# Kernel optimization log

Measured on AMD Instinct MI355X. Metric: run time of the kernel, lower is better.

## Reference

```python
import jax, jax.numpy as jnp
from jax import lax
import numpy as np

B, H, W = 16, 512, 512
NBINS = 256
MARGIN_EYE = 12
BLUR_SIZE = 5
ALPHA_SKIN, ALPHA_EYE, ALPHA_LIP = 0.3, 0.8, 0.1


def de_norm(x):
    return jnp.clip((x + 1.0) * 0.5, 0.0, 1.0)


def renorm(x):
    return x * 2.0 - 1.0


def _match_channel(src, ref, w_s, w_r):
    # src/ref: (P,) pixel values in [0,255]; w_s/w_r: (P,) mask weights
    b_s = jnp.clip(src.astype(jnp.int32), 0, NBINS - 1)
    b_r = jnp.clip(ref.astype(jnp.int32), 0, NBINS - 1)
    h_s = jnp.zeros((NBINS,), src.dtype).at[b_s].add(w_s)   # masked histogram
    h_r = jnp.zeros((NBINS,), ref.dtype).at[b_r].add(w_r)
    cdf_s = jnp.cumsum(h_s) / jnp.maximum(jnp.sum(h_s), 1e-6)
    cdf_r = jnp.cumsum(h_r) / jnp.maximum(jnp.sum(h_r), 1e-6)
    # CDF-matching transfer table (equiv. of cal_trans in PSGAN/EleGANt)
    table = jnp.clip(jnp.searchsorted(cdf_r, cdf_s), 0, NBINS - 1).astype(src.dtype)
    return table[b_s]


def masked_his_match(image_s, image_r, mask_s, mask_r):
    # image: (3,H,W), mask: (1,H,W)
    s = de_norm(image_s) * 255.0 * mask_s
    r = de_norm(image_r) * 255.0 * mask_r
    w_s = mask_s.reshape(-1)
    w_r = mask_r.reshape(-1)
    matched = jax.vmap(_match_channel, in_axes=(0, 0, None, None))(
        s.reshape(3, -1), r.reshape(3, -1), w_s, w_r).reshape(s.shape)
    matched = jnp.where(mask_s > 0, matched, s)  # only masked pixels replaced
    return renorm(matched / 255.0)


def expand_area(mask, margin):
    # morphological dilation (max pool) of (1,H,W) mask
    k = 2 * margin + 1
    return lax.reduce_window(mask, 0.0, lax.max, (1, k, k), (1, 1, 1), 'SAME')


def mask_blur(mask, blur_size):
    # box blur; 'valid' mode: blurred support kept inside original mask
    k = blur_size
    s = lax.reduce_window(mask, 0.0, lax.add, (1, k, k), (1, 1, 1), 'SAME') / float(k * k)
    return s * mask


def generate_pgt(image_s, image_r, mask_s, mask_r, lms_s, lms_r):
    pgt = image_s
    # skin (channel 1)
    m = mask_s[1:2]
    pgt = (1.0 - m) * pgt + m * masked_his_match(image_s, image_r, m, mask_r[1:2])
    # neck (channel 4)
    m = mask_s[4:5]
    pgt = (1.0 - m) * pgt + m * masked_his_match(image_s, image_r, m, mask_r[4:5])
    # lip (channel 0)
    m = mask_s[0:1]
    pgt = (1.0 - m) * pgt + m * masked_his_match(image_s, image_r, m, mask_r[0:1])
    # eyes (channels 2,3), dilated and intersected with skin
    m_se = expand_area(jnp.sum(mask_s[2:4], axis=0, keepdims=True), MARGIN_EYE) * mask_s[1:2]
    m_re = expand_area(jnp.sum(mask_r[2:4], axis=0, keepdims=True), MARGIN_EYE) * mask_r[1:2]
    eye_match = masked_his_match(image_s, image_r, m_se, m_re)
    mb = mask_blur(m_se, BLUR_SIZE)
    pgt = (1.0 - mb) * pgt + mb * eye_match
    # fine_align (reconstructed, simplified: per-region alpha blend of reference,
    # landmark warp omitted -- helper source not provided)
    for m, a in ((mask_s[1:2], ALPHA_SKIN), (m_se, ALPHA_EYE), (mask_s[0:1], ALPHA_LIP)):
        pgt = (1.0 - a * m) * pgt + (a * m) * image_r
    return pgt


def setup_inputs() -> dict:
    key = jax.random.key(0)
    ks = jax.random.split(key, 6)
    sources = jax.random.uniform(ks[0], (B, 3, H, W), jnp.float32, -1.0, 1.0)
    targets = jax.random.uniform(ks[1], (B, 3, H, W), jnp.float32, -1.0, 1.0)
    mask_srcs = (jax.random.uniform(ks[2], (B, 5, H, W)) < 0.3).astype(jnp.float32)
    mask_tars = (jax.random.uniform(ks[3], (B, 5, H, W)) < 0.3).astype(jnp.float32)
    lms_srcs = jax.random.uniform(ks[4], (B, 68, 2), jnp.float32, 0.0, float(H))
    lms_tars = jax.random.uniform(ks[5], (B, 68, 2), jnp.float32, 0.0, float(H))
    return {"sources": sources, "targets": targets, "mask_srcs": mask_srcs,
            "mask_tars": mask_tars, "lms_srcs": lms_srcs, "lms_tars": lms_tars}


def reference(sources, targets, mask_srcs, mask_tars, lms_srcs, lms_tars):
    # vmap over batch replaces the per-sample Python loop of ComposePGT.forward
    return jax.vmap(generate_pgt)(sources, targets, mask_srcs, mask_tars, lms_srcs, lms_tars)
```

## Files before the change

kernel.cpp:

```cpp
#include <hip/hip_runtime.h>
#include <stdint.h>

#define BB 16
#define HH 512
#define WW 512
#define HW (HH*WW)
#define NB 256

#define YC 36
#define SROWS 64
#define MROWS 40
#define NYCH 15


__device__ __forceinline__ float denorm255(float x) {
    return fminf(fmaxf((x + 1.0f) * 0.5f, 0.0f), 1.0f) * 255.0f;
}
__device__ __forceinline__ float renorm_lut(int t) {
    return ((float)t / 255.0f) * 2.0f - 1.0f;
}
__device__ __forceinline__ uint32_t alignb(uint32_t hi, uint32_t lo, int r) {
    return (uint32_t)(((((uint64_t)hi) << 32) | lo) >> (8 * r));
}

__device__ __forceinline__ void hist4(int* h, uint32_t cw,
                                      float4 v0, float4 v1, float4 v2)
{
    float d0[4] = {denorm255(v0.x), denorm255(v0.y), denorm255(v0.z), denorm255(v0.w)};
    float d1[4] = {denorm255(v1.x), denorm255(v1.y), denorm255(v1.z), denorm255(v1.w)};
    float d2[4] = {denorm255(v2.x), denorm255(v2.y), denorm255(v2.z), denorm255(v2.w)};
    #pragma unroll
    for (int j = 0; j < 4; j++) {
        uint32_t pb = (cw >> (8 * j)) & 0xFFu;
        if (pb & 8u) {
            atomicAdd(&h[0 * NB + min((int)d0[j], 255)], 1);
            atomicAdd(&h[1 * NB + min((int)d1[j], 255)], 1);
            atomicAdd(&h[2 * NB + min((int)d2[j], 255)], 1);
        }
        if (pb & 16u) {
            atomicAdd(&h[3 * NB + min((int)d0[j], 255)], 1);
            atomicAdd(&h[4 * NB + min((int)d1[j], 255)], 1);
            atomicAdd(&h[5 * NB + min((int)d2[j], 255)], 1);
        }
        if (pb & 4u) {
            atomicAdd(&h[6 * NB + min((int)d0[j], 255)], 1);
            atomicAdd(&h[7 * NB + min((int)d1[j], 255)], 1);
            atomicAdd(&h[8 * NB + min((int)d2[j], 255)], 1);
        }
        int mei = (int)((pb >> 5) & 3u);
        if (mei) {
            float fm = (float)mei;
            atomicAdd(&h[ 9 * NB + min((int)(d0[j] * fm), 255)], mei);
            atomicAdd(&h[10 * NB + min((int)(d1[j] * fm), 255)], mei);
            atomicAdd(&h[11 * NB + min((int)(d2[j] * fm), 255)], mei);
        }
    }
}

__global__ void __launch_bounds__(256) fused_mask_kernel(
    const float* __restrict__ ms, const float* __restrict__ mr,
    const float* __restrict__ src, const float* __restrict__ tgt,
    uint32_t* __restrict__ C, uint32_t* __restrict__ mbs,
    int* __restrict__ hist)
{
    __shared__ uint32_t sHor[SROWS][128];
    __shared__ uint32_t sMse[MROWS][129];
    __shared__ int h[2][12 * NB];

    int blk  = (blockIdx.x & 7) * 60 + (blockIdx.x >> 3);
    int ych  = blk % NYCH;
    int sb   = blk / NYCH;
    int side = sb >> 4;
    int b    = sb & 15;
    int y0   = ych * YC;

    const float* base = (side ? mr : ms) + (size_t)b * 5 * HW;
    int r0 = threadIdx.x >> 5;
    int c  = threadIdx.x & 31;

    for (int i = threadIdx.x; i < 2 * 12 * NB; i += 256) ((int*)h)[i] = 0;

    for (int it = 0; it < 8; ++it) {
        int L  = r0 + 8 * it;
        int gy = y0 - 14 + L;
        bool inimg = (gy >= 0 && gy < HH);
        bool m1row = inimg && (L >= 12 && L < 52);
        bool owned = inimg && (L >= 14 && L < 50);

        float4 v[5][4];
        #pragma unroll
        for (int p = 0; p < 5; p++)
            #pragma unroll
            for (int j = 0; j < 4; j++) v[p][j] = make_float4(0.f, 0.f, 0.f, 0.f);

        if (inimg) {
            const float* rowp = base + (size_t)gy * WW + 16 * c;
            const float4* p2 = (const float4*)(rowp + 2 * (size_t)HW);
            const float4* p3 = (const float4*)(rowp + 3 * (size_t)HW);
            #pragma unroll
            for (int j = 0; j < 4; j++) { v[2][j] = p2[j]; v[3][j] = p3[j]; }
            if (m1row) {
                const float4* p1 = (const float4*)(rowp + (size_t)HW);
                #pragma unroll
                for (int j = 0; j < 4; j++) v[1][j] = p1[j];
            }
            if (owned) {
                const float4* p0 = (const float4*)(rowp);
                const float4* p4 = (const float4*)(rowp + 4 * (size_t)HW);
                #pragma unroll
                for (int j = 0; j < 4; j++) { v[0][j] = p0[j]; v[4][j] = p4[j]; }
            }
        }

        uint32_t Wd[4], E[4];
        #pragma unroll
        for (int j = 0; j < 4; j++) {
            uint32_t wc = 0;
            #pragma unroll
            for (int k = 0; k < 4; k++) {
                float a0 = (&v[0][j].x)[k];
                float a1 = (&v[1][j].x)[k];
                float a2 = (&v[2][j].x)[k];
                float a3 = (&v[3][j].x)[k];
                float a4 = (&v[4][j].x)[k];
                uint32_t e  = (uint32_t)(a2 + a3);
                uint32_t pb = (a0 > 0.f ? 4u : 0u) | (a1 > 0.f ? 8u : 0u)
                            | (a4 > 0.f ? 16u : 0u);
                wc |= (e | pb) << (8 * k);
            }
            Wd[j] = wc;
            E[j]  = wc & 0x03030303u;
        }

        uint32_t Lw[3], Rw[3];
        #pragma unroll
        for (int i = 0; i < 3; i++) {
            uint32_t lv = __shfl_up(E[i + 1], 1, 32);
            Lw[i] = (c == 0) ? 0u : lv;
            uint32_t rv = __shfl_down(E[i], 1, 32);
            Rw[i] = (c == 31) ? 0u : rv;
        }
        uint32_t arr[10] = {Lw[0], Lw[1], Lw[2], E[0], E[1], E[2], E[3],
                            Rw[0], Rw[1], Rw[2]};
        #pragma unroll
        for (int k = 0; k < 4; k++) {
            const int b3 = 3 + k;
            uint32_t a = arr[b3];
            #pragma unroll
            for (int s = 1; s <= 12; s++) {
                int ai = s >> 2, rrs = s & 3;
                uint32_t vp, vm;
                if (rrs == 0) {
                    vp = arr[b3 + ai];
                    vm = arr[b3 - ai];
                } else {
                    vp = alignb(arr[b3 + ai + 1], arr[b3 + ai], rrs);
                    int am = (s + 3) >> 2;
                    vm = alignb(arr[b3 - am + 1], arr[b3 - am], 4 - rrs);
                }
                a |= vp | vm;
            }
            sHor[L][4 * c + k] = Wd[k] | (a << 5);
        }
    }
    __syncthreads();

    {
        int w  = threadIdx.x & 127;
        int mg = threadIdx.x >> 7;
        for (int k = 0; k < 20; ++k) {
            int m = mg * 20 + k;
            uint32_t o = 0;
            #pragma unroll
            for (int dy = 0; dy < 25; ++dy) o |= sHor[m + dy][w];
            uint32_t vv = (o >> 5) & 0x03030303u;
            uint32_t t3 = vv & (vv >> 1) & 0x01010101u;
            vv -= t3;
            uint32_t m1 = (sHor[m + 12][w] >> 3) & 0x01010101u;
            vv &= m1 * 3u;
            sMse[m][w] = vv;
        }
    }
    __syncthreads();

    {
        int ck = threadIdx.x & 31;
        int rr = threadIdx.x >> 5;
        size_t plane = (size_t)(side * BB + b);
        uint32_t* Cp = C + plane * (HW / 4);
        uint32_t* Mp = mbs + (size_t)b * (HW / 4);
        for (int o = rr; o < YC; o += 8) {
            int gy = y0 + o;
            if (gy >= HH) break;
            uint4 cw;
            #pragma unroll
            for (int q = 0; q < 4; q++) {
                uint32_t b5 = sHor[14 + o][4 * ck + q] & 0x1F1F1F1Fu;
                uint32_t mv = sMse[o + 2][4 * ck + q];
                (&cw.x)[q] = b5 | (mv << 5);
            }
            *((uint4*)(Cp + (size_t)gy * 128 + 4 * ck)) = cw;

            if (side == 0) {
                uint32_t s[6] = {0u, 0u, 0u, 0u, 0u, 0u};
                #pragma unroll
                for (int dy = 0; dy < 5; dy++) {
                    const uint32_t* rp = sMse[o + dy];
                    if (ck > 0)  s[0] += rp[4 * ck - 1];
                    s[1] += rp[4 * ck + 0];
                    s[2] += rp[4 * ck + 1];
                    s[3] += rp[4 * ck + 2];
                    s[4] += rp[4 * ck + 3];
                    if (ck < 31) s[5] += rp[4 * ck + 4];
                }
                uint4 ob;
                #pragma unroll
                for (int k = 0; k < 4; k++) {
                    uint32_t vv = s[k + 1];
                    vv += alignb(s[k + 1], s[k],     2);
                    vv += alignb(s[k + 1], s[k],     3);
                    vv += alignb(s[k + 2], s[k + 1], 1);
                    vv += alignb(s[k + 2], s[k + 1], 2);
                    (&ob.x)[k] = vv;
                }
                *((uint4*)(Mp + (size_t)gy * 128 + 4 * ck)) = ob;
            }
        }
    }

    {
        int* hw = h[threadIdx.x >> 7];
        const float* img = (side ? tgt : src) + (size_t)b * 3 * HW;
        const float4* i0 = (const float4*)(img);
        const float4* i1 = (const float4*)(img + HW);
        const float4* i2 = (const float4*)(img + 2 * (size_t)HW);
        for (int idx = threadIdx.x; idx < YC * 64; idx += 256) {
            int o = idx >> 6, g = idx & 63;
            int gy = y0 + o;
            if (gy >= HH) continue;
            int cidx = gy * 64 + g;
            uint32_t cwx = (sHor[14 + o][2 * g]     & 0x1F1F1F1Fu)
                         | (sMse[o + 2][2 * g]     << 5);
            uint32_t cwy = (sHor[14 + o][2 * g + 1] & 0x1F1F1F1Fu)
                         | (sMse[o + 2][2 * g + 1] << 5);
            float4 a0 = i0[2 * cidx], b0v = i0[2 * cidx + 1];
            float4 a1 = i1[2 * cidx], b1v = i1[2 * cidx + 1];
            float4 a2 = i2[2 * cidx], b2v = i2[2 * cidx + 1];
            hist4(hw, cwx, a0, a1, a2);
            hist4(hw, cwy, b0v, b1v, b2v);
        }
    }
    __syncthreads();
    {
        int* gh = hist + (size_t)(b * 2 + side) * 12 * NB;
        for (int i = threadIdx.x; i < 12 * NB; i += 256) {
            int s = h[0][i] + h[1][i];
            if (s) atomicAdd(&gh[i], s);
        }
    }
}

__global__ void __launch_bounds__(NB) table_kernel(
    const int* __restrict__ hist, uint8_t* __restrict__ table)
{
    int idx = blockIdx.x;
    int c = idx % 3; int rest = idx / 3; int rg = rest & 3; int b = rest >> 2;
    const int* hs = hist + ((size_t)((b * 2 + 0) * 4 + rg) * 3 + c) * NB;
    const int* hr = hist + ((size_t)((b * 2 + 1) * 4 + rg) * 3 + c) * NB;
    __shared__ int a[NB];
    __shared__ float cr[NB];
    int t = threadIdx.x;

    a[t] = hs[t];
    __syncthreads();
    for (int off = 1; off < NB; off <<= 1) {
        int v = (t >= off) ? a[t - off] : 0;
        __syncthreads();
        a[t] += v;
        __syncthreads();
    }
    int totS = a[NB - 1];
    int cumS = a[t];
    __syncthreads();

    a[t] = hr[t];
    __syncthreads();
    for (int off = 1; off < NB; off <<= 1) {
        int v = (t >= off) ? a[t - off] : 0;
        __syncthreads();
        a[t] += v;
        __syncthreads();
    }
    int totR = a[NB - 1];
    cr[t] = (float)a[t] / fmaxf((float)totR, 1e-6f);
    float v = (float)cumS / fmaxf((float)totS, 1e-6f);
    __syncthreads();

    int cnt = 0;
    for (int j = 0; j < NB; j++) cnt += (cr[j] < v) ? 1 : 0;
    table[(size_t)idx * NB + t] = (uint8_t)min(cnt, 255);
}

__device__ __forceinline__ void proc4(uint32_t cw, uint32_t qw,
    float4 x0, float4 x1, float4 x2, float4 r0, float4 r1, float4 r2,
    const uint8_t* tb, float4& o0, float4& o1, float4& o2)
{
    float X0[4] = {x0.x, x0.y, x0.z, x0.w};
    float X1[4] = {x1.x, x1.y, x1.z, x1.w};
    float X2[4] = {x2.x, x2.y, x2.z, x2.w};
    float R0[4] = {r0.x, r0.y, r0.z, r0.w};
    float R1[4] = {r1.x, r1.y, r1.z, r1.w};
    float R2[4] = {r2.x, r2.y, r2.z, r2.w};
    #pragma unroll
    for (int j = 0; j < 4; j++) {
        uint32_t pb = (cw >> (8 * j)) & 0xFFu;
        float q = (float)((qw >> (8 * j)) & 0xFFu);
        float m0f = (float)((pb >> 2) & 1u);
        float m1f = (float)((pb >> 3) & 1u);
        float m4f = (float)((pb >> 4) & 1u);
        float fm  = (float)((pb >> 5) & 3u);
        float d0 = denorm255(X0[j]), d1 = denorm255(X1[j]), d2 = denorm255(X2[j]);
        float p0 = X0[j], p1 = X1[j], p2 = X2[j];
        {
            float e0 = renorm_lut(tb[0 * NB + min((int)(d0 * m1f), 255)]);
            float e1 = renorm_lut(tb[1 * NB + min((int)(d1 * m1f), 255)]);
            float e2 = renorm_lut(tb[2 * NB + min((int)(d2 * m1f), 255)]);
            p0 = (1.0f - m1f) * p0 + m1f * e0;
            p1 = (1.0f - m1f) * p1 + m1f * e1;
            p2 = (1.0f - m1f) * p2 + m1f * e2;
        }
        {
            float e0 = renorm_lut(tb[3 * NB + min((int)(d0 * m4f), 255)]);
            float e1 = renorm_lut(tb[4 * NB + min((int)(d1 * m4f), 255)]);
            float e2 = renorm_lut(tb[5 * NB + min((int)(d2 * m4f), 255)]);
            p0 = (1.0f - m4f) * p0 + m4f * e0;
            p1 = (1.0f - m4f) * p1 + m4f * e1;
            p2 = (1.0f - m4f) * p2 + m4f * e2;
        }
        {
            float e0 = renorm_lut(tb[6 * NB + min((int)(d0 * m0f), 255)]);
            float e1 = renorm_lut(tb[7 * NB + min((int)(d1 * m0f), 255)]);
            float e2 = renorm_lut(tb[8 * NB + min((int)(d2 * m0f), 255)]);
            p0 = (1.0f - m0f) * p0 + m0f * e0;
            p1 = (1.0f - m0f) * p1 + m0f * e1;
            p2 = (1.0f - m0f) * p2 + m0f * e2;
        }
        {
            float mb = (q * (1.0f / 25.0f)) * fm;
            float e0 = renorm_lut(tb[ 9 * NB + min((int)(d0 * fm), 255)]);
            float e1 = renorm_lut(tb[10 * NB + min((int)(d1 * fm), 255)]);
            float e2 = renorm_lut(tb[11 * NB + min((int)(d2 * fm), 255)]);
            p0 = (1.0f - mb) * p0 + mb * e0;
            p1 = (1.0f - mb) * p1 + mb * e1;
            p2 = (1.0f - mb) * p2 + mb * e2;
        }
        float a = 0.3f * m1f;
        p0 = (1.0f - a) * p0 + a * R0[j];
        p1 = (1.0f - a) * p1 + a * R1[j];
        p2 = (1.0f - a) * p2 + a * R2[j];
        a = 0.8f * fm;
        p0 = (1.0f - a) * p0 + a * R0[j];
        p1 = (1.0f - a) * p1 + a * R1[j];
        p2 = (1.0f - a) * p2 + a * R2[j];
        a = 0.1f * m0f;
        p0 = (1.0f - a) * p0 + a * R0[j];
        p1 = (1.0f - a) * p1 + a * R1[j];
        p2 = (1.0f - a) * p2 + a * R2[j];
        (&o0.x)[j] = p0; (&o1.x)[j] = p1; (&o2.x)[j] = p2;
    }
}

__global__ void __launch_bounds__(256) compose_kernel(
    const float* __restrict__ src, const float* __restrict__ tgt,
    const uint32_t* __restrict__ C, const uint32_t* __restrict__ mbs,
    const uint8_t* __restrict__ table, float* __restrict__ out)
{
    int t = blockIdx.x * 256 + threadIdx.x;
    int b = t >> 15;
    int c = t & 32767;

    __shared__ uint8_t tb[12 * NB];
    {
        const uint32_t* gt = (const uint32_t*)(table + (size_t)b * 12 * NB);
        uint32_t* tw = (uint32_t*)tb;
        for (int i = threadIdx.x; i < 12 * NB / 4; i += 256) tw[i] = gt[i];
    }
    __syncthreads();

    const float4* s0 = (const float4*)(src + (size_t)b * 3 * HW);
    const float4* s1 = s0 + HW / 4;
    const float4* s2 = s1 + HW / 4;
    const float4* t0 = (const float4*)(tgt + (size_t)b * 3 * HW);
    const float4* t1 = t0 + HW / 4;
    const float4* t2 = t1 + HW / 4;
    const uint2* pc = (const uint2*)(C + (size_t)b * (HW / 4));
    const uint2* qc = (const uint2*)(mbs + (size_t)b * (HW / 4));
    float4* o0 = (float4*)(out + (size_t)b * 3 * HW);
    float4* o1 = o0 + HW / 4;
    float4* o2 = o1 + HW / 4;

    uint2 cw = pc[c];
    uint2 qw = qc[c];
    float4 xa0 = s0[2 * c], xb0 = s0[2 * c + 1];
    float4 xa1 = s1[2 * c], xb1 = s1[2 * c + 1];
    float4 xa2 = s2[2 * c], xb2 = s2[2 * c + 1];
    float4 ra0 = t0[2 * c], rb0 = t0[2 * c + 1];
    float4 ra1 = t1[2 * c], rb1 = t1[2 * c + 1];
    float4 ra2 = t2[2 * c], rb2 = t2[2 * c + 1];

    float4 oa0, oa1, oa2, ob0, ob1, ob2;
    proc4(cw.x, qw.x, xa0, xa1, xa2, ra0, ra1, ra2, tb, oa0, oa1, oa2);
    proc4(cw.y, qw.y, xb0, xb1, xb2, rb0, rb1, rb2, tb, ob0, ob1, ob2);

    o0[2 * c] = oa0; o0[2 * c + 1] = ob0;
    o1[2 * c] = oa1; o1[2 * c + 1] = ob1;
    o2[2 * c] = oa2; o2[2 * c + 1] = ob2;
}

extern "C" void kernel_launch(void* const* d_in, const int* in_sizes, int n_in,
                              void* d_out, int out_size, void* d_ws, size_t ws_size,
                              hipStream_t stream) {
    const float* src = (const float*)d_in[0];
    const float* tgt = (const float*)d_in[1];
    const float* ms  = (const float*)d_in[2];
    const float* mr  = (const float*)d_in[3];
    float* out = (float*)d_out;

    uint8_t* ws = (uint8_t*)d_ws;
    uint32_t* C   = (uint32_t*)(ws);
    uint32_t* mbs = (uint32_t*)(ws + (size_t)4 * BB * HW);
    int* hist     = (int*)(ws + (size_t)5 * BB * HW);
    uint8_t* table = ws + (size_t)5 * BB * HW + (size_t)2 * BB * 12 * NB * 4;

    hipMemsetAsync(hist, 0, (size_t)2 * BB * 12 * NB * sizeof(int), stream);

    fused_mask_kernel<<<2 * BB * NYCH, 256, 0, stream>>>(ms, mr, src, tgt, C, mbs, hist);
    table_kernel<<<BB * 4 * 3, NB, 0, stream>>>(hist, table);
    compose_kernel<<<BB * (HW / 8) / 256, 256, 0, stream>>>(src, tgt, C, mbs, table, out);
}
```

Baseline: 327.3 us.

## Software-pipeline image loads for histogram with inline-asm prefetch across barriers

Image float4 loads for the histogram phase are now issued with inline-asm global_load_dwordx4, before the vertical mask pass. They are double-buffered across the nine histogram steps using explicit vmcnt waits, so global-load latency overlaps with the LDS dilation work. The histogram phase moves ahead of the C/mask-blur write phase. __syncthreads is replaced by raw s_barrier with lgkmcnt waits. sMse padding changes so rows can be read as uint2. This adds register pressure and relies on hand-counted vmcnt values, which is fragile if the compiler inserts other memory ops.

Measured after the change: 334.9 us. 2.3% more time.

```diff
diff --git a/kernel.cpp b/kernel.cpp
--- a/kernel.cpp
+++ b/kernel.cpp
@@ -10,7 +10,10 @@
 #define YC 36
 #define SROWS 64
 #define MROWS 40
+#define MPAD 132
 #define NYCH 15
+
+typedef float f32x4 __attribute__((ext_vector_type(4)));
 
 
 __device__ __forceinline__ float denorm255(float x) {
@@ -24,35 +27,35 @@
 }
 
 __device__ __forceinline__ void hist4(int* h, uint32_t cw,
-                                      float4 v0, float4 v1, float4 v2)
+                                      f32x4 v0, f32x4 v1, f32x4 v2)
 {
-    float d0[4] = {denorm255(v0.x), denorm255(v0.y), denorm255(v0.z), denorm255(v0.w)};
-    float d1[4] = {denorm255(v1.x), denorm255(v1.y), denorm255(v1.z), denorm255(v1.w)};
-    float d2[4] = {denorm255(v2.x), denorm255(v2.y), denorm255(v2.z), denorm255(v2.w)};
     #pragma unroll
     for (int j = 0; j < 4; j++) {
         uint32_t pb = (cw >> (8 * j)) & 0xFFu;
+        float d0 = denorm255(v0[j]);
+        float d1 = denorm255(v1[j]);
+        float d2 = denorm255(v2[j]);
         if (pb & 8u) {
-            atomicAdd(&h[0 * NB + min((int)d0[j], 255)], 1);
-            atomicAdd(&h[1 * NB + min((int)d1[j], 255)], 1);
-            atomicAdd(&h[2 * NB + min((int)d2[j], 255)], 1);
+            atomicAdd(&h[0 * NB + min((int)d0, 255)], 1);
+            atomicAdd(&h[1 * NB + min((int)d1, 255)], 1);
+            atomicAdd(&h[2 * NB + min((int)d2, 255)], 1);
         }
         if (pb & 16u) {
-            atomicAdd(&h[3 * NB + min((int)d0[j], 255)], 1);
-            atomicAdd(&h[4 * NB + min((int)d1[j], 255)], 1);
-            atomicAdd(&h[5 * NB + min((int)d2[j], 255)], 1);
+            atomicAdd(&h[3 * NB + min((int)d0, 255)], 1);
+            atomicAdd(&h[4 * NB + min((int)d1, 255)], 1);
+            atomicAdd(&h[5 * NB + min((int)d2, 255)], 1);
         }
         if (pb & 4u) {
-            atomicAdd(&h[6 * NB + min((int)d0[j], 255)], 1);
-            atomicAdd(&h[7 * NB + min((int)d1[j], 255)], 1);
-            atomicAdd(&h[8 * NB + min((int)d2[j], 255)], 1);
+            atomicAdd(&h[6 * NB + min((int)d0, 255)], 1);
+            atomicAdd(&h[7 * NB + min((int)d1, 255)], 1);
+            atomicAdd(&h[8 * NB + min((int)d2, 255)], 1);
         }
         int mei = (int)((pb >> 5) & 3u);
         if (mei) {
             float fm = (float)mei;
-            atomicAdd(&h[ 9 * NB + min((int)(d0[j] * fm), 255)], mei);
-            atomicAdd(&h[10 * NB + min((int)(d1[j] * fm), 255)], mei);
-            atomicAdd(&h[11 * NB + min((int)(d2[j] * fm), 255)], mei);
+            atomicAdd(&h[ 9 * NB + min((int)(d0 * fm), 255)], mei);
+            atomicAdd(&h[10 * NB + min((int)(d1 * fm), 255)], mei);
+            atomicAdd(&h[11 * NB + min((int)(d2 * fm), 255)], mei);
         }
     }
 }
@@ -64,7 +67,7 @@
     int* __restrict__ hist)
 {
     __shared__ uint32_t sHor[SROWS][128];
-    __shared__ uint32_t sMse[MROWS][129];
+    __shared__ uint32_t sMse[MROWS][MPAD];
     __shared__ int h[2][12 * NB];
 
     int blk  = (blockIdx.x & 7) * 60 + (blockIdx.x >> 3);
@@ -77,6 +80,18 @@
     const float* base = (side ? mr : ms) + (size_t)b * 5 * HW;
     int r0 = threadIdx.x >> 5;
     int c  = threadIdx.x & 31;
+
+    int* hw = h[threadIdx.x >> 7];
+    const float* img = (side ? tgt : src) + (size_t)b * 3 * HW;
+    const float4* i0 = (const float4*)(img);
+    const float4* i1 = (const float4*)(img + HW);
+    const float4* i2 = (const float4*)(img + 2 * (size_t)HW);
+    auto cidx_of = [&](int it) -> int {
+        int idx = threadIdx.x + it * 256;
+        int o = idx >> 6, g = idx & 63;
+        int gyc = min(y0 + o, HH - 1);
+        return gyc * 64 + g;
+    };
 
     for (int i = threadIdx.x; i < 2 * 12 * NB; i += 256) ((int*)h)[i] = 0;
 
@@ -163,7 +178,25 @@
             sHor[L][4 * c + k] = Wd[k] | (a << 5);
         }
     }
-    __syncthreads();
+
+    f32x4 A0, A1, A2, A3, A4, A5, B0, B1, B2, B3, B4, B5;
+#define ISSUE(CIDX, R0, R1, R2, R3, R4, R5) do {                              \
+    int _ci = (CIDX);                                                         \
+    const float* _p0 = (const float*)(i0 + 2 * _ci);                          \
+    const float* _p1 = (const float*)(i1 + 2 * _ci);                          \
+    const float* _p2 = (const float*)(i2 + 2 * _ci);                          \
+    asm volatile("global_load_dwordx4 %0, %1, off"           : "=v"(R0) : "v"(_p0)); \
+    asm volatile("global_load_dwordx4 %0, %1, off offset:16" : "=v"(R1) : "v"(_p0)); \
+    asm volatile("global_load_dwordx4 %0, %1, off"           : "=v"(R2) : "v"(_p1)); \
+    asm volatile("global_load_dwordx4 %0, %1, off offset:16" : "=v"(R3) : "v"(_p1)); \
+    asm volatile("global_load_dwordx4 %0, %1, off"           : "=v"(R4) : "v"(_p2)); \
+    asm volatile("global_load_dwordx4 %0, %1, off offset:16" : "=v"(R5) : "v"(_p2)); \
+} while (0)
+    ISSUE(cidx_of(0), A0, A1, A2, A3, A4, A5);
+    ISSUE(cidx_of(1), B0, B1, B2, B3, B4, B5);
+
+    asm volatile("s_waitcnt lgkmcnt(0)" ::: "memory");
+    __builtin_amdgcn_s_barrier();
 
     {
         int w  = threadIdx.x & 127;
@@ -181,7 +214,33 @@
             sMse[m][w] = vv;
         }
     }
-    __syncthreads();
+    asm volatile("s_waitcnt lgkmcnt(0)" ::: "memory");
+    __builtin_amdgcn_s_barrier();
+
+#define STEP(IT, WAITN, R0, R1, R2, R3, R4, R5) do {                          \
+    asm volatile("s_waitcnt vmcnt(" WAITN ")" ::: "memory");                  \
+    __builtin_amdgcn_sched_barrier(0);                                        \
+    int _idx = threadIdx.x + (IT) * 256;                                      \
+    int _o = _idx >> 6, _g = _idx & 63;                                       \
+    if (y0 + _o < HH) {                                                       \
+        uint2 hv = *(const uint2*)&sHor[14 + _o][2 * _g];                     \
+        uint2 mv = *(const uint2*)&sMse[_o + 2][2 * _g];                      \
+        hist4(hw, (hv.x & 0x1F1F1F1Fu) | (mv.x << 5), R0, R2, R4);            \
+        hist4(hw, (hv.y & 0x1F1F1F1Fu) | (mv.y << 5), R1, R3, R5);            \
+    }                                                                         \
+    if ((IT) + 2 < 9) ISSUE(cidx_of((IT) + 2), R0, R1, R2, R3, R4, R5);       \
+} while (0)
+    STEP(0, "6", A0, A1, A2, A3, A4, A5);
+    STEP(1, "6", B0, B1, B2, B3, B4, B5);
+    STEP(2, "6", A0, A1, A2, A3, A4, A5);
+    STEP(3, "6", B0, B1, B2, B3, B4, B5);
+    STEP(4, "6", A0, A1, A2, A3, A4, A5);
+    STEP(5, "6", B0, B1, B2, B3, B4, B5);
+    STEP(6, "6", A0, A1, A2, A3, A4, A5);
+    STEP(7, "6", B0, B1, B2, B3, B4, B5);
+    STEP(8, "0", A0, A1, A2, A3, A4, A5);
+#undef STEP
+#undef ISSUE
 
     {
         int ck = threadIdx.x & 31;
@@ -228,29 +287,8 @@
         }
     }
 
-    {
-        int* hw = h[threadIdx.x >> 7];
-        const float* img = (side ? tgt : src) + (size_t)b * 3 * HW;
-        const float4* i0 = (const float4*)(img);
-        const float4* i1 = (const float4*)(img + HW);
-        const float4* i2 = (const float4*)(img + 2 * (size_t)HW);
-        for (int idx = threadIdx.x; idx < YC * 64; idx += 256) {
-            int o = idx >> 6, g = idx & 63;
-            int gy = y0 + o;
-            if (gy >= HH) continue;
-            int cidx = gy * 64 + g;
-            uint32_t cwx = (sHor[14 + o][2 * g]     & 0x1F1F1F1Fu)
-                         | (sMse[o + 2][2 * g]     << 5);
-            uint32_t cwy = (sHor[14 + o][2 * g + 1] & 0x1F1F1F1Fu)
-                         | (sMse[o + 2][2 * g + 1] << 5);
-            float4 a0 = i0[2 * cidx], b0v = i0[2 * cidx + 1];
-            float4 a1 = i1[2 * cidx], b1v = i1[2 * cidx + 1];
-            float4 a2 = i2[2 * cidx], b2v = i2[2 * cidx + 1];
-            hist4(hw, cwx, a0, a1, a2);
-            hist4(hw, cwy, b0v, b1v, b2v);
-        }
-    }
-    __syncthreads();
+    asm volatile("s_waitcnt lgkmcnt(0)" ::: "memory");
+    __builtin_amdgcn_s_barrier();
     {
         int* gh = hist + (size_t)(b * 2 + side) * 12 * NB;
         for (int i = threadIdx.x; i < 12 * NB; i += 256) {
```

## Halve row chunk per block and use single shared histogram for higher occupancy

Applied to the files above, without the earlier changes.

Cuts the rows each block owns from 36 to 18, so there are twice as many blocks (29 chunks per plane), and shrinks the shared arrays to match. The two per-half histogram copies are merged into one shared histogram, and sMse is padded to 132 so the mask words can be read as aligned uint2 loads. The aim is lower LDS use per block for better occupancy and balance, and fewer registers by denormalising pixel values lazily. The cost is a larger relative halo (the 14-row margin is recomputed more often) and more atomic contention on the single histogram.

Measured after the change: 331.7 us. No clear change (+1.3%).

```diff
diff --git a/kernel.cpp b/kernel.cpp
--- a/kernel.cpp
+++ b/kernel.cpp
@@ -7,10 +7,11 @@
 #define HW (HH*WW)
 #define NB 256
 
-#define YC 36
-#define SROWS 64
-#define MROWS 40
-#define NYCH 15
+#define YC 18
+#define SROWS 46
+#define MROWS 22
+#define MPAD 132
+#define NYCH 29
 
 
 __device__ __forceinline__ float denorm255(float x) {
@@ -26,33 +27,33 @@
 __device__ __forceinline__ void hist4(int* h, uint32_t cw,
                                       float4 v0, float4 v1, float4 v2)
 {
-    float d0[4] = {denorm255(v0.x), denorm255(v0.y), denorm255(v0.z), denorm255(v0.w)};
-    float d1[4] = {denorm255(v1.x), denorm255(v1.y), denorm255(v1.z), denorm255(v1.w)};
-    float d2[4] = {denorm255(v2.x), denorm255(v2.y), denorm255(v2.z), denorm255(v2.w)};
     #pragma unroll
     for (int j = 0; j < 4; j++) {
         uint32_t pb = (cw >> (8 * j)) & 0xFFu;
+        float d0 = denorm255((&v0.x)[j]);
+        float d1 = denorm255((&v1.x)[j]);
+        float d2 = denorm255((&v2.x)[j]);
         if (pb & 8u) {
-            atomicAdd(&h[0 * NB + min((int)d0[j], 255)], 1);
-            atomicAdd(&h[1 * NB + min((int)d1[j], 255)], 1);
-            atomicAdd(&h[2 * NB + min((int)d2[j], 255)], 1);
+            atomicAdd(&h[0 * NB + min((int)d0, 255)], 1);
+            atomicAdd(&h[1 * NB + min((int)d1, 255)], 1);
+            atomicAdd(&h[2 * NB + min((int)d2, 255)], 1);
         }
         if (pb & 16u) {
-            atomicAdd(&h[3 * NB + min((int)d0[j], 255)], 1);
-            atomicAdd(&h[4 * NB + min((int)d1[j], 255)], 1);
-            atomicAdd(&h[5 * NB + min((int)d2[j], 255)], 1);
+            atomicAdd(&h[3 * NB + min((int)d0, 255)], 1);
+            atomicAdd(&h[4 * NB + min((int)d1, 255)], 1);
+            atomicAdd(&h[5 * NB + min((int)d2, 255)], 1);
         }
         if (pb & 4u) {
-            atomicAdd(&h[6 * NB + min((int)d0[j], 255)], 1);
-            atomicAdd(&h[7 * NB + min((int)d1[j], 255)], 1);
-            atomicAdd(&h[8 * NB + min((int)d2[j], 255)], 1);
+            atomicAdd(&h[6 * NB + min((int)d0, 255)], 1);
+            atomicAdd(&h[7 * NB + min((int)d1, 255)], 1);
+            atomicAdd(&h[8 * NB + min((int)d2, 255)], 1);
         }
         int mei = (int)((pb >> 5) & 3u);
         if (mei) {
             float fm = (float)mei;
-            atomicAdd(&h[ 9 * NB + min((int)(d0[j] * fm), 255)], mei);
-            atomicAdd(&h[10 * NB + min((int)(d1[j] * fm), 255)], mei);
-            atomicAdd(&h[11 * NB + min((int)(d2[j] * fm), 255)], mei);
+            atomicAdd(&h[ 9 * NB + min((int)(d0 * fm), 255)], mei);
+            atomicAdd(&h[10 * NB + min((int)(d1 * fm), 255)], mei);
+            atomicAdd(&h[11 * NB + min((int)(d2 * fm), 255)], mei);
         }
     }
 }
@@ -64,10 +65,10 @@
     int* __restrict__ hist)
 {
     __shared__ uint32_t sHor[SROWS][128];
-    __shared__ uint32_t sMse[MROWS][129];
-    __shared__ int h[2][12 * NB];
-
-    int blk  = (blockIdx.x & 7) * 60 + (blockIdx.x >> 3);
+    __shared__ uint32_t sMse[MROWS][MPAD];
+    __shared__ int h[12 * NB];
+
+    int blk  = (blockIdx.x & 7) * 116 + (blockIdx.x >> 3);
     int ych  = blk % NYCH;
     int sb   = blk / NYCH;
     int side = sb >> 4;
@@ -78,14 +79,15 @@
     int r0 = threadIdx.x >> 5;
     int c  = threadIdx.x & 31;
 
-    for (int i = threadIdx.x; i < 2 * 12 * NB; i += 256) ((int*)h)[i] = 0;
-
-    for (int it = 0; it < 8; ++it) {
+    for (int i = threadIdx.x; i < 12 * NB; i += 256) h[i] = 0;
+
+    for (int it = 0; it < 6; ++it) {
         int L  = r0 + 8 * it;
+        if (L >= SROWS) break;
         int gy = y0 - 14 + L;
         bool inimg = (gy >= 0 && gy < HH);
-        bool m1row = inimg && (L >= 12 && L < 52);
-        bool owned = inimg && (L >= 14 && L < 50);
+        bool m1row = inimg && (L >= 12 && L < 34);
+        bool owned = inimg && (L >= 14 && L < 32);
 
         float4 v[5][4];
         #pragma unroll
@@ -168,8 +170,8 @@
     {
         int w  = threadIdx.x & 127;
         int mg = threadIdx.x >> 7;
-        for (int k = 0; k < 20; ++k) {
-            int m = mg * 20 + k;
+        for (int k = 0; k < 11; ++k) {
+            int m = mg * 11 + k;
             uint32_t o = 0;
             #pragma unroll
             for (int dy = 0; dy < 25; ++dy) o |= sHor[m + dy][w];
@@ -229,32 +231,31 @@
     }
 
     {
-        int* hw = h[threadIdx.x >> 7];
         const float* img = (side ? tgt : src) + (size_t)b * 3 * HW;
         const float4* i0 = (const float4*)(img);
         const float4* i1 = (const float4*)(img + HW);
         const float4* i2 = (const float4*)(img + 2 * (size_t)HW);
-        for (int idx = threadIdx.x; idx < YC * 64; idx += 256) {
+        for (int it = 0; it < 5; ++it) {
+            int idx = threadIdx.x + it * 256;
+            if (idx >= YC * 64) break;
             int o = idx >> 6, g = idx & 63;
             int gy = y0 + o;
             if (gy >= HH) continue;
             int cidx = gy * 64 + g;
-            uint32_t cwx = (sHor[14 + o][2 * g]     & 0x1F1F1F1Fu)
-                         | (sMse[o + 2][2 * g]     << 5);
-            uint32_t cwy = (sHor[14 + o][2 * g + 1] & 0x1F1F1F1Fu)
-                         | (sMse[o + 2][2 * g + 1] << 5);
+            uint2 hv = *(const uint2*)&sHor[14 + o][2 * g];
+            uint2 mv = *(const uint2*)&sMse[o + 2][2 * g];
             float4 a0 = i0[2 * cidx], b0v = i0[2 * cidx + 1];
             float4 a1 = i1[2 * cidx], b1v = i1[2 * cidx + 1];
             float4 a2 = i2[2 * cidx], b2v = i2[2 * cidx + 1];
-            hist4(hw, cwx, a0, a1, a2);
-            hist4(hw, cwy, b0v, b1v, b2v);
+            hist4(h, (hv.x & 0x1F1F1F1Fu) | (mv.x << 5), a0, a1, a2);
+            hist4(h, (hv.y & 0x1F1F1F1Fu) | (mv.y << 5), b0v, b1v, b2v);
         }
     }
     __syncthreads();
     {
         int* gh = hist + (size_t)(b * 2 + side) * 12 * NB;
         for (int i = threadIdx.x; i < 12 * NB; i += 256) {
-            int s = h[0][i] + h[1][i];
+            int s = h[i];
             if (s) atomicAdd(&gh[i], s);
         }
     }
```
